# Kernel optimization log

Hardware: AMD Instinct MI355X
Metric: run time of the kernel (lower is better)

## Reference

```python
import jax, jax.numpy as jnp
import numpy as np

TAU = 0.1
LAMBD = 0.75
EPS = 1e-8  # torch cosine_similarity norm clamp


def setup_inputs() -> dict:
    key = jax.random.key(0)
    k1, k2 = jax.random.split(key)
    B, D = 8192, 768
    v = jax.random.normal(k1, (B, D), dtype=jnp.float32)
    u = jax.random.normal(k2, (B, D), dtype=jnp.float32)
    return {"v": v, "u": u}


def reference(v, u):
    # Batched equivalent of the per-sample Python loop:
    # cos(v_i, u_j) = <v_i/||v_i||, u_j/||u_j||>, with torch's eps clamp on norms.
    v = v.astype(jnp.float32)
    u = u.astype(jnp.float32)
    vn = v / jnp.maximum(jnp.linalg.norm(v, axis=1, keepdims=True), EPS)
    un = u / jnp.maximum(jnp.linalg.norm(u, axis=1, keepdims=True), EPS)
    sim = jnp.einsum('id,jd->ij', vn, un) / TAU  # [B, B] logits
    diag = jnp.diagonal(sim)
    # image->text: -log( exp(sim_ii) / sum_j exp(sim_ij) )
    loss_it = jax.nn.logsumexp(sim, axis=1) - diag
    # text->image: -log( exp(sim_ii) / sum_j exp(sim_ji) )
    loss_ti = jax.nn.logsumexp(sim, axis=0) - diag
    # In the torch source text_image calls .item(), detaching it from autograd.
    loss_ti = jax.lax.stop_gradient(loss_ti)
    return jnp.mean(LAMBD * loss_it + (1.0 - LAMBD) * loss_ti)
```

## Files before the change

kernel.cpp:

```cpp
#include <hip/hip_runtime.h>
#include <hip/hip_bf16.h>

typedef unsigned char u8;
typedef unsigned short u16;
typedef unsigned int u32;
typedef float f32x16 __attribute__((ext_vector_type(16)));
typedef float f32x2 __attribute__((ext_vector_type(2)));
typedef int i32x4 __attribute__((ext_vector_type(4)));
typedef int i32x8 __attribute__((ext_vector_type(8)));

#define B_SZ 8192
#define D_SZ 768
#define TAU_INV 10.0f
#define ESCALE 0.014088818758681283f
#define FP4_SCALE 32.0f
#define SCHRAU_K1 118185.58f
#define SCHRAU_K2 1064879685.0f


__device__ __forceinline__ u32 fp4_enc(float x) {
    float y = fabsf(x);
    u32 n = (u32)(y >= 0.25f) + (u32)(y >= 0.75f) + (u32)(y >= 1.25f) +
            (u32)(y >= 1.75f) + (u32)(y >= 2.5f)  + (u32)(y >= 3.5f) +
            (u32)(y >= 5.0f);
    return n | (x < 0.f ? 8u : 0u);
}

__device__ __forceinline__ u16 fp4_pack4(float x, float y, float z, float w) {
    return (u16)(fp4_enc(x) | (fp4_enc(y) << 4) | (fp4_enc(z) << 8) | (fp4_enc(w) << 12));
}

__global__ __launch_bounds__(256) void norm_kernel(const float4* __restrict__ v,
                                                   const float4* __restrict__ u,
                                                   u16* __restrict__ vn,
                                                   u16* __restrict__ un,
                                                   float* __restrict__ diag) {
    const int wid = threadIdx.x >> 6, lane = threadIdx.x & 63;
    const int row = blockIdx.x * 4 + wid;
    const float4* vr = v + (size_t)row * 192;
    const float4* ur = u + (size_t)row * 192;
    float4 a[3], b[3];
    float sv = 0.f, su = 0.f, sd = 0.f;
#pragma unroll
    for (int c = 0; c < 3; ++c) {
        a[c] = vr[lane + 64 * c];
        b[c] = ur[lane + 64 * c];
        sv += a[c].x * a[c].x + a[c].y * a[c].y + a[c].z * a[c].z + a[c].w * a[c].w;
        su += b[c].x * b[c].x + b[c].y * b[c].y + b[c].z * b[c].z + b[c].w * b[c].w;
        sd += a[c].x * b[c].x + a[c].y * b[c].y + a[c].z * b[c].z + a[c].w * b[c].w;
    }
#pragma unroll
    for (int m = 1; m < 64; m <<= 1) {
        sv += __shfl_xor(sv, m);
        su += __shfl_xor(su, m);
        sd += __shfl_xor(sd, m);
    }
    const float iv = FP4_SCALE / fmaxf(sqrtf(sv), 1e-8f);
    const float iu = FP4_SCALE / fmaxf(sqrtf(su), 1e-8f);
    const int rg = row >> 5, rr = row & 31;
#pragma unroll
    for (int c = 0; c < 3; ++c) {
        u16 pa = fp4_pack4(a[c].x * iv, a[c].y * iv, a[c].z * iv, a[c].w * iv);
        u16 pb = fp4_pack4(b[c].x * iu, b[c].y * iu, b[c].z * iu, b[c].w * iu);
        const int e = lane + 64 * c;
        const int idx = (rg * 12 + (e >> 4)) * 512 + ((e >> 3) & 1) * 256 + rr * 8 + (e & 7);
        vn[idx] = pa;
        un[idx] = pb;
    }
    if (lane == 0) diag[row] = sd * iv * iu * TAU_INV / (FP4_SCALE * FP4_SCALE);
}

__device__ __forceinline__ i32x8 ldfrag4(const u8* __restrict__ base, u32 off) {
    i32x4 lo = *(const i32x4*)(base + off);
    return __builtin_shufflevector(lo, lo, 0, 1, 2, 3, -1, -1, -1, -1);
}

__device__ __forceinline__ f32x16 mx_mfma4(i32x8 a, i32x8 b, f32x16 c) {
    return __builtin_amdgcn_mfma_scale_f32_32x32x64_f8f6f4(
        a, b, c, 4, 4, 0, 0x7F7F7F7F, 0, 0x7F7F7F7F);
}

__global__ __launch_bounds__(256, 4) void simexp_kernel(const u8* __restrict__ vn,
                                                        const u8* __restrict__ un,
                                                        float* __restrict__ rowP,
                                                        float* __restrict__ colP) {
    __shared__ float rowLds[2][128];
    __shared__ float colLds[2][128];

    const int tid  = threadIdx.x;
    const int wid  = tid >> 6;
    const int lane = tid & 63;
    const int l32  = lane & 31;
    const int h    = lane >> 5;
    const int wr = wid >> 1, wc = wid & 1;

    const int id = blockIdx.x;
    const int chunk = id >> 6;
    const int li = id & 63;
    const int rb = ((chunk >> 3) << 3) + (li >> 3);
    const int cb = ((chunk & 7) << 3) + (li & 7);

    const int aBase = __builtin_amdgcn_readfirstlane((rb * 4 + wr * 2) * 12288);
    const int bBase = __builtin_amdgcn_readfirstlane((cb * 4 + wc * 2) * 12288);
    const u8* __restrict__ A0 = vn + aBase;
    const u8* __restrict__ A1 = A0 + 12288;
    const u8* __restrict__ B0 = un + bBase;
    const u8* __restrict__ B1 = B0 + 12288;
    u32 voff = (u32)lane * 16;

    f32x16 acc[2][2];
#pragma unroll
    for (int i = 0; i < 2; ++i)
#pragma unroll
        for (int j = 0; j < 2; ++j)
#pragma unroll
            for (int r = 0; r < 16; ++r) acc[i][j][r] = 0.f;

    i32x8 fa[2][2], fb[2][2];

#define LOAD_SLOT(s)                        \
    {                                       \
        fa[s][0] = ldfrag4(A0, voff);       \
        fa[s][1] = ldfrag4(A1, voff);       \
        fb[s][0] = ldfrag4(B0, voff);       \
        fb[s][1] = ldfrag4(B1, voff);       \
        voff += 1024;                       \
    }
#define MFMA_SLOT(s)                                          \
    {                                                         \
        __builtin_amdgcn_s_setprio(1);                        \
        acc[0][0] = mx_mfma4(fa[s][0], fb[s][0], acc[0][0]);  \
        acc[1][0] = mx_mfma4(fa[s][1], fb[s][0], acc[1][0]);  \
        acc[0][1] = mx_mfma4(fa[s][0], fb[s][1], acc[0][1]);  \
        acc[1][1] = mx_mfma4(fa[s][1], fb[s][1], acc[1][1]);  \
        __builtin_amdgcn_s_setprio(0);                        \
    }

    LOAD_SLOT(0)
#pragma unroll 1
    for (int it = 0; it < 12; it += 2) {
        LOAD_SLOT(1)
        MFMA_SLOT(0)
        if (it + 2 < 12) LOAD_SLOT(0)
        MFMA_SLOT(1)
    }

    f32x2 val2[16];
    f32x2 cacc2[2];
#pragma unroll
    for (int p = 0; p < 16; ++p) { val2[p].x = 0.f; val2[p].y = 0.f; }
    cacc2[0].x = 0.f; cacc2[0].y = 0.f;
    cacc2[1].x = 0.f; cacc2[1].y = 0.f;
#pragma unroll
    for (int i = 0; i < 2; ++i)
#pragma unroll
        for (int j = 0; j < 2; ++j)
#pragma unroll
            for (int r = 0; r < 16; r += 2) {
                f32x2 a;
                a.x = acc[i][j][r];
                a.y = acc[i][j][r + 1];
                f32x2 t = a * SCHRAU_K1 + SCHRAU_K2;
                f32x2 e;
                e.x = __int_as_float((int)t.x);
                e.y = __int_as_float((int)t.y);
                val2[i * 8 + (r >> 1)] += e;
                cacc2[j] += e;
            }

#pragma unroll
    for (int m = 16; m >= 2; m >>= 1) {
        const int n = m >> 1;
        const bool hi = (l32 & m) != 0;
#pragma unroll
        for (int p = 0; p < n; ++p) {
            f32x2 a = val2[p], b = val2[p + n];
            f32x2 x, y;
            x.x = hi ? b.x : a.x;  x.y = hi ? b.y : a.y;
            y.x = hi ? a.x : b.x;  y.y = hi ? a.y : b.y;
            f32x2 s;
            s.x = __shfl_xor(y.x, m);
            s.y = __shfl_xor(y.y, m);
            val2[p] = x + s;
        }
    }
    {
        f32x2 s;
        s.x = __shfl_xor(val2[0].x, 1);
        s.y = __shfl_xor(val2[0].y, 1);
        val2[0] += s;
    }
    {
        const int q = (l32 >> 1) & 15;
        const int t = 2 * q + (l32 & 1);
        const int i = t >> 4, r = t & 15;
        const int row = wr * 64 + i * 32 + (r & 3) + 8 * (r >> 2) + 4 * h;
        rowLds[wc][row] = (l32 & 1) ? val2[0].y : val2[0].x;
    }
    {
        float c0 = cacc2[0].x + cacc2[0].y;
        float c1 = cacc2[1].x + cacc2[1].y;
        c0 += __shfl_xor(c0, 32);
        c1 += __shfl_xor(c1, 32);
        if (h == 0) {
            colLds[wr][wc * 64 + l32]      = c0;
            colLds[wr][wc * 64 + 32 + l32] = c1;
        }
    }
    __syncthreads();
    if (tid < 128) {
        rowP[(size_t)cb * B_SZ + rb * 128 + tid] = rowLds[0][tid] + rowLds[1][tid];
    } else {
        const int t = tid - 128;
        colP[(size_t)rb * B_SZ + cb * 128 + t] = colLds[0][t] + colLds[1][t];
    }
}

__global__ __launch_bounds__(256) void finalize_kernel(const float* __restrict__ rowP,
                                                       const float* __restrict__ colP,
                                                       const float* __restrict__ diag,
                                                       float* __restrict__ out) {
    const int i = blockIdx.x * 256 + threadIdx.x;
    float rs = 0.f, cs = 0.f;
#pragma unroll 8
    for (int p = 0; p < 64; ++p) {
        rs += rowP[(size_t)p * B_SZ + i];
        cs += colP[(size_t)p * B_SZ + i];
    }
    float contrib = (0.75f * logf(rs) + 0.25f * logf(cs) - diag[i]) * (1.0f / (float)B_SZ);
#pragma unroll
    for (int m = 1; m < 64; m <<= 1) contrib += __shfl_xor(contrib, m);
    __shared__ float red[4];
    const int wid = threadIdx.x >> 6, lane = threadIdx.x & 63;
    if (lane == 0) red[wid] = contrib;
    __syncthreads();
    if (threadIdx.x == 0) atomicAdd(out, red[0] + red[1] + red[2] + red[3]);
}

extern "C" void kernel_launch(void* const* d_in, const int* in_sizes, int n_in,
                              void* d_out, int out_size, void* d_ws, size_t ws_size,
                              hipStream_t stream) {
    const float* v = (const float*)d_in[0];
    const float* u = (const float*)d_in[1];
    char* ws = (char*)d_ws;
    u16* vn4   = (u16*)(ws);
    u16* un4   = (u16*)(ws + 3145728);
    float* dg  = (float*)(ws + 6291456);
    float* rwp = (float*)(ws + 6324224);
    float* clp = (float*)(ws + 8421376);
    float* out = (float*)d_out;

    hipMemsetAsync(out, 0, sizeof(float), stream);
    hipLaunchKernelGGL(norm_kernel, dim3(2048), dim3(256), 0, stream,
                       (const float4*)v, (const float4*)u, vn4, un4, dg);
    hipLaunchKernelGGL(simexp_kernel, dim3(4096), dim3(256), 0, stream,
                       (const u8*)vn4, (const u8*)un4, rwp, clp);
    hipLaunchKernelGGL(finalize_kernel, dim3(B_SZ / 256), dim3(256), 0, stream, rwp, clp, dg, out);
}
```

Before: 131.3 us.

## Stage FP4 operand tiles through LDS with 256x256 blocks of 16 waves

The similarity kernel moves from 128x128 tiles of 4 waves, where each wave loaded its own fragments straight from global memory, to 256x256 tiles of 16 waves. Each wave streams one 32-row panel into a triple-buffered LDS stage using global_load_lds, and all waves read their MFMA fragments from LDS. This cuts redundant global and L2 traffic through shared reuse and halves the partial-sum buffers that finalize reads. The cost is a block-wide barrier per K step and larger blocks, which reduces the number of resident blocks and the latency hiding between independent blocks.

```diff
diff --git a/kernel.cpp b/kernel.cpp
--- a/kernel.cpp
+++ b/kernel.cpp
@@ -70,9 +70,14 @@
     if (lane == 0) diag[row] = sd * iv * iu * TAU_INV / (FP4_SCALE * FP4_SCALE);
 }
 
-__device__ __forceinline__ i32x8 ldfrag4(const u8* __restrict__ base, u32 off) {
-    i32x4 lo = *(const i32x4*)(base + off);
+__device__ __forceinline__ i32x8 ldsfrag(const u8* p) {
+    i32x4 lo = *(const i32x4*)p;
     return __builtin_shufflevector(lo, lo, 0, 1, 2, 3, -1, -1, -1, -1);
+}
+
+__device__ __forceinline__ void gload_lds16(const u8* g, u8* l) {
+    __builtin_amdgcn_global_load_lds((const __attribute__((address_space(1))) void*)g,
+                                     (__attribute__((address_space(3))) void*)l, 16, 0, 0);
 }
 
 __device__ __forceinline__ f32x16 mx_mfma4(i32x8 a, i32x8 b, f32x16 c) {
@@ -80,33 +85,30 @@
         a, b, c, 4, 4, 0, 0x7F7F7F7F, 0, 0x7F7F7F7F);
 }
 
-__global__ __launch_bounds__(256, 4) void simexp_kernel(const u8* __restrict__ vn,
-                                                        const u8* __restrict__ un,
-                                                        float* __restrict__ rowP,
-                                                        float* __restrict__ colP) {
-    __shared__ float rowLds[2][128];
-    __shared__ float colLds[2][128];
+__global__ __launch_bounds__(1024, 4) void simexp_kernel(const u8* __restrict__ vn,
+                                                         const u8* __restrict__ un,
+                                                         float* __restrict__ rowP,
+                                                         float* __restrict__ colP) {
+    __shared__ __attribute__((aligned(16))) u8 stg[3][16][1024];
+    __shared__ float rowLds[4][256];
+    __shared__ float colLds[4][256];
 
     const int tid  = threadIdx.x;
-    const int wid  = tid >> 6;
+    const int w    = tid >> 6;
     const int lane = tid & 63;
     const int l32  = lane & 31;
     const int h    = lane >> 5;
-    const int wr = wid >> 1, wc = wid & 1;
+    const int wr = w >> 2, wc = w & 3;
 
     const int id = blockIdx.x;
     const int chunk = id >> 6;
     const int li = id & 63;
-    const int rb = ((chunk >> 3) << 3) + (li >> 3);
-    const int cb = ((chunk & 7) << 3) + (li & 7);
-
-    const int aBase = __builtin_amdgcn_readfirstlane((rb * 4 + wr * 2) * 12288);
-    const int bBase = __builtin_amdgcn_readfirstlane((cb * 4 + wc * 2) * 12288);
-    const u8* __restrict__ A0 = vn + aBase;
-    const u8* __restrict__ A1 = A0 + 12288;
-    const u8* __restrict__ B0 = un + bBase;
-    const u8* __restrict__ B1 = B0 + 12288;
-    u32 voff = (u32)lane * 16;
+    const int rb = ((chunk >> 2) << 3) + (li >> 3);
+    const int cb = ((chunk & 3) << 3) + (li & 7);
+
+    const u8* gsrc = (w < 8 ? vn + (size_t)(rb * 8 + w) * 12288
+                            : un + (size_t)(cb * 8 + (w - 8)) * 12288)
+                     + (u32)lane * 16;
 
     f32x16 acc[2][2];
 #pragma unroll
@@ -116,34 +118,30 @@
 #pragma unroll
             for (int r = 0; r < 16; ++r) acc[i][j][r] = 0.f;
 
-    i32x8 fa[2][2], fb[2][2];
-
-#define LOAD_SLOT(s)                        \
-    {                                       \
-        fa[s][0] = ldfrag4(A0, voff);       \
-        fa[s][1] = ldfrag4(A1, voff);       \
-        fb[s][0] = ldfrag4(B0, voff);       \
-        fb[s][1] = ldfrag4(B1, voff);       \
-        voff += 1024;                       \
-    }
-#define MFMA_SLOT(s)                                          \
-    {                                                         \
-        __builtin_amdgcn_s_setprio(1);                        \
-        acc[0][0] = mx_mfma4(fa[s][0], fb[s][0], acc[0][0]);  \
-        acc[1][0] = mx_mfma4(fa[s][1], fb[s][0], acc[1][0]);  \
-        acc[0][1] = mx_mfma4(fa[s][0], fb[s][1], acc[0][1]);  \
-        acc[1][1] = mx_mfma4(fa[s][1], fb[s][1], acc[1][1]);  \
-        __builtin_amdgcn_s_setprio(0);                        \
-    }
-
-    LOAD_SLOT(0)
-#pragma unroll 1
-    for (int it = 0; it < 12; it += 2) {
-        LOAD_SLOT(1)
-        MFMA_SLOT(0)
-        if (it + 2 < 12) LOAD_SLOT(0)
-        MFMA_SLOT(1)
-    }
+#define STAGE(t) gload_lds16(gsrc + (t) * 1024, &stg[(t) % 3][w][0]);
+
+    STAGE(0)
+    STAGE(1)
+    asm volatile("s_waitcnt vmcnt(1)\n\ts_barrier" ::: "memory");
+
+#pragma unroll
+    for (int t = 0; t < 12; ++t) {
+        if (t + 2 < 12) STAGE(t + 2)
+        const u8* base = &stg[t % 3][0][0] + (u32)lane * 16;
+        i32x8 fa0 = ldsfrag(base + (wr * 2)     * 1024);
+        i32x8 fa1 = ldsfrag(base + (wr * 2 + 1) * 1024);
+        i32x8 fb0 = ldsfrag(base + (8 + wc * 2) * 1024);
+        i32x8 fb1 = ldsfrag(base + (9 + wc * 2) * 1024);
+        __builtin_amdgcn_s_setprio(1);
+        acc[0][0] = mx_mfma4(fa0, fb0, acc[0][0]);
+        acc[1][0] = mx_mfma4(fa1, fb0, acc[1][0]);
+        acc[0][1] = mx_mfma4(fa0, fb1, acc[0][1]);
+        acc[1][1] = mx_mfma4(fa1, fb1, acc[1][1]);
+        __builtin_amdgcn_s_setprio(0);
+        if (t < 10)       asm volatile("s_waitcnt vmcnt(1)\n\ts_barrier" ::: "memory");
+        else if (t == 10) asm volatile("s_waitcnt vmcnt(0)\n\ts_barrier" ::: "memory");
+    }
+#undef STAGE
 
     f32x2 val2[16];
     f32x2 cacc2[2];
@@ -208,11 +206,13 @@
         }
     }
     __syncthreads();
-    if (tid < 128) {
-        rowP[(size_t)cb * B_SZ + rb * 128 + tid] = rowLds[0][tid] + rowLds[1][tid];
-    } else {
-        const int t = tid - 128;
-        colP[(size_t)rb * B_SZ + cb * 128 + t] = colLds[0][t] + colLds[1][t];
+    if (tid < 256) {
+        rowP[(size_t)cb * B_SZ + rb * 256 + tid] =
+            rowLds[0][tid] + rowLds[1][tid] + rowLds[2][tid] + rowLds[3][tid];
+    } else if (tid < 512) {
+        const int t = tid - 256;
+        colP[(size_t)rb * B_SZ + cb * 256 + t] =
+            colLds[0][t] + colLds[1][t] + colLds[2][t] + colLds[3][t];
     }
 }
 
@@ -223,7 +223,7 @@
     const int i = blockIdx.x * 256 + threadIdx.x;
     float rs = 0.f, cs = 0.f;
 #pragma unroll 8
-    for (int p = 0; p < 64; ++p) {
+    for (int p = 0; p < 32; ++p) {
         rs += rowP[(size_t)p * B_SZ + i];
         cs += colP[(size_t)p * B_SZ + i];
     }
@@ -247,13 +247,13 @@
     u16* un4   = (u16*)(ws + 3145728);
     float* dg  = (float*)(ws + 6291456);
     float* rwp = (float*)(ws + 6324224);
-    float* clp = (float*)(ws + 8421376);
+    float* clp = (float*)(ws + 7372800);
     float* out = (float*)d_out;
 
     hipMemsetAsync(out, 0, sizeof(float), stream);
     hipLaunchKernelGGL(norm_kernel, dim3(2048), dim3(256), 0, stream,
                        (const float4*)v, (const float4*)u, vn4, un4, dg);
-    hipLaunchKernelGGL(simexp_kernel, dim3(4096), dim3(256), 0, stream,
+    hipLaunchKernelGGL(simexp_kernel, dim3(1024), dim3(1024), 0, stream,
                        (const u8*)vn4, (const u8*)un4, rwp, clp);
     hipLaunchKernelGGL(finalize_kernel, dim3(B_SZ / 256), dim3(256), 0, stream, rwp, clp, dg, out);
 }
```

Result: faster. 125.5 us (-4.5%).
